# Kernel optimization log

Hardware: AMD Instinct MI355X
Metric: run time of the kernel (lower is better)

## Reference

```python
import jax, jax.numpy as jnp
import numpy as np

B, S, D = 2, 2048, 1024
H, HD = 16, 64

def setup_inputs() -> dict:
    key = jax.random.key(0)
    k1, k2, k3 = jax.random.split(key, 3)
    x = jax.random.normal(k1, (B, S, D), dtype=jnp.float32)
    w_qkv = jax.random.normal(k2, (3 * D, D), dtype=jnp.float32) * (D ** -0.5)
    w_out = jax.random.normal(k3, (D, D), dtype=jnp.float32) * (D ** -0.5)
    return {"x": x, "w_qkv": w_qkv, "w_out": w_out}

def reference(x, w_qkv, w_out):
    scale = HD ** -0.5
    # qkv projection: torch Linear applies x @ W.T
    qkv = jnp.einsum('bsd,ed->bse', x, w_qkv)            # [B,S,3D]
    qkv = qkv.reshape(B, S, 3, H, HD)
    q, k, v = qkv[:, :, 0], qkv[:, :, 1], qkv[:, :, 2]   # [B,S,H,HD]
    # scores: explicit matmul-softmax-matmul (unfused, as in source)
    scores = jnp.einsum('bqhd,bkhd->bhqk', q, k) * scale  # [B,H,S,S]
    attn = jax.nn.softmax(scores, axis=-1)
    out = jnp.einsum('bhqk,bkhd->bqhd', attn, v)          # [B,S,H,HD]
    out = out.reshape(B, S, D)
    return jnp.einsum('bsd,ed->bse', out, w_out)
```

## Files before the change

### kernel.cpp

```cpp
#include <hip/hip_runtime.h>
#include <math.h>

#define B_ 2
#define S_ 2048
#define D_ 1024
#define H_ 16
#define HD_ 64

typedef short bf16x8 __attribute__((ext_vector_type(8)));
typedef short bf16x4 __attribute__((ext_vector_type(4)));
typedef float f32x4 __attribute__((ext_vector_type(4)));

#define MFMA32(a, b, c) __builtin_amdgcn_mfma_f32_16x16x32_bf16(a, b, c, 0, 0, 0)
#define MFMA16(a, b, c) __builtin_amdgcn_mfma_f32_16x16x16bf16_1k(a, b, c, 0, 0, 0)

static __device__ __forceinline__ unsigned short f2bf(float f) {
    union { float f; unsigned u; } v = {f};
    return (unsigned short)((v.u + 0x7fffu + ((v.u >> 16) & 1u)) >> 16);
}

static __device__ __forceinline__ void gl2lds16(const void* g, void* l) {
    __builtin_amdgcn_global_load_lds((const __attribute__((address_space(1))) unsigned int*)g,
                                     (__attribute__((address_space(3))) unsigned int*)l,
                                     16, 0, 0);
}

__global__ __launch_bounds__(256) void cvt_all(const float* __restrict__ x,
                                               const float* __restrict__ wq,
                                               const float* __restrict__ wo,
                                               unsigned short* __restrict__ xb,
                                               unsigned short* __restrict__ wqb,
                                               unsigned short* __restrict__ wob) {
    const int N0 = 1048576, N1 = 786432, N2 = 262144;
    int stride = gridDim.x * blockDim.x;
    for (int i = blockIdx.x * blockDim.x + threadIdx.x; i < N0 + N1 + N2; i += stride) {
        const float4* src; ushort4* dst; int j;
        if (i < N0)            { src = (const float4*)x;  dst = (ushort4*)xb;  j = i; }
        else if (i < N0 + N1)  { src = (const float4*)wq; dst = (ushort4*)wqb; j = i - N0; }
        else                   { src = (const float4*)wo; dst = (ushort4*)wob; j = i - N0 - N1; }
        float4 v = src[j];
        ushort4 o;
        o.x = f2bf(v.x); o.y = f2bf(v.y); o.z = f2bf(v.z); o.w = f2bf(v.w);
        dst[j] = o;
    }
}

template <int BN>
__global__ __launch_bounds__(256) void gemm_nt_b(const unsigned short* __restrict__ A,
                                                 const unsigned short* __restrict__ Bm,
                                                 void* __restrict__ Cout,
                                                 int M, int N, int K, int c_bf16) {
    constexpr int BM = 128, BK = 32;
    constexpr int MI = (BN == 128) ? 4 : 2;
    constexpr int NI = 4;
    constexpr int SEGS = (BM + BN) / 16;
    __shared__ unsigned short As[BM * BK];
    __shared__ unsigned short Bs[BN * BK];

    const int tid = threadIdx.x;
    const int wave = tid >> 6, lane = tid & 63;
    const int m16 = lane & 15, quad = lane >> 4;
    const int wrow = (BN == 128) ? (wave >> 1) * 64 : wave * 32;
    const int wcol = (BN == 128) ? (wave & 1) * 64 : 0;
    const int row0 = blockIdx.y * BM, col0 = blockIdx.x * BN;

    const int lrow = lane >> 2;
    const int lk = (lane & 3) * 8;

    f32x4 acc[MI][NI] = {};

    for (int k0 = 0; k0 < K; k0 += BK) {
        __syncthreads();
        for (int s = wave; s < SEGS; s += 4) {
            if (s < BM / 16) {
                gl2lds16(&A[(size_t)(row0 + s * 16 + lrow) * K + k0 + lk],
                         &As[s * 16 * BK]);
            } else {
                int t = s - BM / 16;
                gl2lds16(&Bm[(size_t)(col0 + t * 16 + lrow) * K + k0 + lk],
                         &Bs[t * 16 * BK]);
            }
        }
        __asm__ volatile("s_waitcnt vmcnt(0)" ::: "memory");
        __syncthreads();

        bf16x8 af[MI], bfr[NI];
        #pragma unroll
        for (int mi = 0; mi < MI; ++mi)
            af[mi] = *(const bf16x8*)&As[(wrow + mi * 16 + m16) * BK + quad * 8];
        #pragma unroll
        for (int ni = 0; ni < NI; ++ni)
            bfr[ni] = *(const bf16x8*)&Bs[(wcol + ni * 16 + m16) * BK + quad * 8];
        #pragma unroll
        for (int mi = 0; mi < MI; ++mi)
            #pragma unroll
            for (int ni = 0; ni < NI; ++ni)
                acc[mi][ni] = MFMA32(af[mi], bfr[ni], acc[mi][ni]);
    }

    #pragma unroll
    for (int mi = 0; mi < MI; ++mi) {
        #pragma unroll
        for (int r = 0; r < 4; ++r) {
            size_t grow = row0 + wrow + mi * 16 + quad * 4 + r;
            #pragma unroll
            for (int ni = 0; ni < NI; ++ni) {
                size_t gcol = col0 + wcol + ni * 16 + m16;
                if (c_bf16)
                    ((unsigned short*)Cout)[grow * N + gcol] = f2bf(acc[mi][ni][r]);
                else
                    ((float*)Cout)[grow * N + gcol] = acc[mi][ni][r];
            }
        }
    }
}

__global__ __launch_bounds__(256) void attn_mfma(const unsigned short* __restrict__ qkv,
                                                 unsigned short* __restrict__ out) {
    constexpr int LDK = 72;
    __shared__ unsigned short Ks[2][64 * LDK];
    __shared__ unsigned short Vt[2][64 * LDK];

    const int id = blockIdx.x;
    const int bh = ((id >> 3) & 3) * 8 + (id & 7);
    const int b = bh >> 4, h = bh & 15;
    const int q0 = (id >> 5) * 64;

    const int tid = threadIdx.x;
    const int wave = tid >> 6, lane = tid & 63;
    const int m16 = lane & 15, quad = lane >> 4;

    const float C1 = 0.125f * 1.44269504089f;
    const float C2 = 10.0f * 1.44269504089f;

    const unsigned short* qrow =
        qkv + ((size_t)b * S_ + q0 + wave * 16 + m16) * (3 * D_) + h * HD_;
    bf16x8 qf0 = *(const bf16x8*)(qrow + quad * 8);
    bf16x8 qf1 = *(const bf16x8*)(qrow + 32 + quad * 8);

    f32x4 o[4] = {};
    f32x4 ol = {0.f, 0.f, 0.f, 0.f};
    const bf16x4 onesf = {(short)0x3F80, (short)0x3F80, (short)0x3F80, (short)0x3F80};

    const unsigned short* kbase = qkv + (size_t)b * S_ * 3 * D_ + D_ + h * HD_;
    const unsigned short* vbase = qkv + (size_t)b * S_ * 3 * D_ + 2 * D_ + h * HD_;

    const int kr = tid >> 3;
    const int kc8 = (tid & 7) * 8;
    const int vrp = (tid >> 4) * 2;
    const int vc4 = (tid & 15) * 4;
    const int vxr = 4 * ((tid & 15) & 7);

    int vaddr[4][4];
    #pragma unroll
    for (int dt = 0; dt < 4; ++dt) {
        int d = dt * 16 + m16;
        int xr = 4 * ((d >> 2) & 7);
        #pragma unroll
        for (int nt = 0; nt < 4; ++nt)
            vaddr[dt][nt] = d * LDK + ((nt * 16 + quad * 4) ^ xr);
    }

    uint4 kg[2];
    ushort4 vg[2][2];

    #pragma unroll
    for (int i = 0; i < 2; ++i) {
        kg[i] = *(const uint4*)(kbase + (size_t)(kr + i * 32) * 3 * D_ + kc8);
        vg[i][0] = *(const ushort4*)(vbase + (size_t)(vrp + i * 32) * 3 * D_ + vc4);
        vg[i][1] = *(const ushort4*)(vbase + (size_t)(vrp + i * 32 + 1) * 3 * D_ + vc4);
    }
    #pragma unroll
    for (int i = 0; i < 2; ++i) {
        *(uint4*)&Ks[0][(kr + i * 32) * LDK + kc8] = kg[i];
        int koff = (vrp + i * 32) ^ vxr;
        *(unsigned*)&Vt[0][(vc4 + 0) * LDK + koff] = (unsigned)vg[i][0].x | ((unsigned)vg[i][1].x << 16);
        *(unsigned*)&Vt[0][(vc4 + 1) * LDK + koff] = (unsigned)vg[i][0].y | ((unsigned)vg[i][1].y << 16);
        *(unsigned*)&Vt[0][(vc4 + 2) * LDK + koff] = (unsigned)vg[i][0].z | ((unsigned)vg[i][1].z << 16);
        *(unsigned*)&Vt[0][(vc4 + 3) * LDK + koff] = (unsigned)vg[i][0].w | ((unsigned)vg[i][1].w << 16);
    }
    __syncthreads();

    for (int t = 0; t < S_ / 64; ++t) {
        const int buf = t & 1;
        const bool more = (t + 1) < (S_ / 64);

        if (more) {
            const size_t kt1 = (size_t)(t + 1) * 64;
            #pragma unroll
            for (int i = 0; i < 2; ++i) {
                kg[i] = *(const uint4*)(kbase + (kt1 + kr + i * 32) * 3 * D_ + kc8);
                vg[i][0] = *(const ushort4*)(vbase + (kt1 + vrp + i * 32) * 3 * D_ + vc4);
                vg[i][1] = *(const ushort4*)(vbase + (kt1 + vrp + i * 32 + 1) * 3 * D_ + vc4);
            }
        }

        bf16x4 pf[4];
        #pragma unroll
        for (int nt = 0; nt < 4; ++nt) {
            const unsigned short* kp = &Ks[buf][(nt * 16 + m16) * LDK];
            bf16x8 kf0 = *(const bf16x8*)(kp + quad * 8);
            bf16x8 kf1 = *(const bf16x8*)(kp + 32 + quad * 8);
            f32x4 z = {0.f, 0.f, 0.f, 0.f};
            z = MFMA32(kf0, qf0, z);
            z = MFMA32(kf1, qf1, z);
            float p0 = __builtin_amdgcn_exp2f(z[0] * C1 - C2);
            float p1 = __builtin_amdgcn_exp2f(z[1] * C1 - C2);
            float p2 = __builtin_amdgcn_exp2f(z[2] * C1 - C2);
            float p3 = __builtin_amdgcn_exp2f(z[3] * C1 - C2);
            union { float f; unsigned u; } u0 = {p0}, u1 = {p1}, u2 = {p2}, u3 = {p3};
            unsigned lo = __builtin_amdgcn_perm(u1.u + 0x8000u, u0.u + 0x8000u, 0x07060302u);
            unsigned hi = __builtin_amdgcn_perm(u3.u + 0x8000u, u2.u + 0x8000u, 0x07060302u);
            union { unsigned u[2]; bf16x4 v; } pk;
            pk.u[0] = lo; pk.u[1] = hi;
            pf[nt] = pk.v;
            ol = MFMA16(pf[nt], onesf, ol);
        }

        #pragma unroll
        for (int nt = 0; nt < 4; ++nt)
            #pragma unroll
            for (int dt = 0; dt < 4; ++dt) {
                bf16x4 vf = *(const bf16x4*)&Vt[buf][vaddr[dt][nt]];
                o[dt] = MFMA16(pf[nt], vf, o[dt]);
            }

        if (more) {
            #pragma unroll
            for (int i = 0; i < 2; ++i) {
                *(uint4*)&Ks[buf ^ 1][(kr + i * 32) * LDK + kc8] = kg[i];
                int koff = (vrp + i * 32) ^ vxr;
                *(unsigned*)&Vt[buf ^ 1][(vc4 + 0) * LDK + koff] = (unsigned)vg[i][0].x | ((unsigned)vg[i][1].x << 16);
                *(unsigned*)&Vt[buf ^ 1][(vc4 + 1) * LDK + koff] = (unsigned)vg[i][0].y | ((unsigned)vg[i][1].y << 16);
                *(unsigned*)&Vt[buf ^ 1][(vc4 + 2) * LDK + koff] = (unsigned)vg[i][0].z | ((unsigned)vg[i][1].z << 16);
                *(unsigned*)&Vt[buf ^ 1][(vc4 + 3) * LDK + koff] = (unsigned)vg[i][0].w | ((unsigned)vg[i][1].w << 16);
            }
        }
        __syncthreads();
    }

    #pragma unroll
    for (int r = 0; r < 4; ++r) {
        float inv = 1.f / ol[r];
        size_t row = (size_t)b * S_ + q0 + wave * 16 + quad * 4 + r;
        unsigned short* op = out + row * D_ + h * HD_;
        #pragma unroll
        for (int dt = 0; dt < 4; ++dt)
            op[dt * 16 + m16] = f2bf(o[dt][r] * inv);
    }
}

extern "C" void kernel_launch(void* const* d_in, const int* in_sizes, int n_in,
                              void* d_out, int out_size, void* d_ws, size_t ws_size,
                              hipStream_t stream) {
    const float* x     = (const float*)d_in[0];
    const float* w_qkv = (const float*)d_in[1];
    const float* w_out = (const float*)d_in[2];
    float* out = (float*)d_out;

    const size_t n_x = (size_t)B_ * S_ * D_;
    const size_t n_wqkv = (size_t)3 * D_ * D_;
    const size_t n_wout = (size_t)D_ * D_;

    unsigned short* xb    = (unsigned short*)d_ws;
    unsigned short* wqkvb = xb + n_x;
    unsigned short* woutb = wqkvb + n_wqkv;
    unsigned short* qkvb  = woutb + n_wout;
    unsigned short* attnb = qkvb + (size_t)B_ * S_ * 3 * D_;

    dim3 blk(256);

    cvt_all<<<2048, blk, 0, stream>>>(x, w_qkv, w_out, xb, wqkvb, woutb);

    gemm_nt_b<128><<<dim3(3 * D_ / 128, B_ * S_ / 128), blk, 0, stream>>>(
        xb, wqkvb, qkvb, B_ * S_, 3 * D_, D_, 1);

    attn_mfma<<<1024, blk, 0, stream>>>(qkvb, attnb);

    gemm_nt_b<64><<<dim3(D_ / 64, B_ * S_ / 128), blk, 0, stream>>>(
        attnb, woutb, out, B_ * S_, D_, D_, 0);
}
```

Baseline: 214.9 us.

## Load K fragments directly from global memory into registers, skipping LDS staging

The attention kernel drops the shared-memory K tile and has each wave load its K MFMA fragments straight from global memory into registers at the start of every iteration. This removes the LDS writes and reads for K and shrinks shared-memory use. The cost is that all four waves in a block redundantly fetch the same K rows, and those loads are no longer prefetched a tile ahead, so their latency sits directly in front of the QK MFMAs. The P-to-bf16 packing also switches from a hand-written perm trick to the HIP __float22bfloat162_rn intrinsic.

```diff
diff --git a/kernel.cpp b/kernel.cpp
--- a/kernel.cpp
+++ b/kernel.cpp
@@ -1,4 +1,5 @@
 #include <hip/hip_runtime.h>
+#include <hip/hip_bf16.h>
 #include <math.h>
 
 #define B_ 2
@@ -17,6 +18,13 @@
 static __device__ __forceinline__ unsigned short f2bf(float f) {
     union { float f; unsigned u; } v = {f};
     return (unsigned short)((v.u + 0x7fffu + ((v.u >> 16) & 1u)) >> 16);
+}
+
+static __device__ __forceinline__ unsigned pk2bf(float a, float b) {
+    __hip_bfloat162 h = __float22bfloat162_rn(make_float2(a, b));
+    unsigned r;
+    __builtin_memcpy(&r, &h, 4);
+    return r;
 }
 
 static __device__ __forceinline__ void gl2lds16(const void* g, void* l) {
@@ -118,7 +126,6 @@
 __global__ __launch_bounds__(256) void attn_mfma(const unsigned short* __restrict__ qkv,
                                                  unsigned short* __restrict__ out) {
     constexpr int LDK = 72;
-    __shared__ unsigned short Ks[2][64 * LDK];
     __shared__ unsigned short Vt[2][64 * LDK];
 
     const int id = blockIdx.x;
@@ -145,8 +152,8 @@
     const unsigned short* kbase = qkv + (size_t)b * S_ * 3 * D_ + D_ + h * HD_;
     const unsigned short* vbase = qkv + (size_t)b * S_ * 3 * D_ + 2 * D_ + h * HD_;
 
-    const int kr = tid >> 3;
-    const int kc8 = (tid & 7) * 8;
+    const unsigned short* kfp = kbase + (size_t)m16 * (3 * D_) + quad * 8;
+
     const int vrp = (tid >> 4) * 2;
     const int vc4 = (tid & 15) * 4;
     const int vxr = 4 * ((tid & 15) & 7);
@@ -161,18 +168,15 @@
             vaddr[dt][nt] = d * LDK + ((nt * 16 + quad * 4) ^ xr);
     }
 
-    uint4 kg[2];
     ushort4 vg[2][2];
 
     #pragma unroll
     for (int i = 0; i < 2; ++i) {
-        kg[i] = *(const uint4*)(kbase + (size_t)(kr + i * 32) * 3 * D_ + kc8);
         vg[i][0] = *(const ushort4*)(vbase + (size_t)(vrp + i * 32) * 3 * D_ + vc4);
         vg[i][1] = *(const ushort4*)(vbase + (size_t)(vrp + i * 32 + 1) * 3 * D_ + vc4);
     }
     #pragma unroll
     for (int i = 0; i < 2; ++i) {
-        *(uint4*)&Ks[0][(kr + i * 32) * LDK + kc8] = kg[i];
         int koff = (vrp + i * 32) ^ vxr;
         *(unsigned*)&Vt[0][(vc4 + 0) * LDK + koff] = (unsigned)vg[i][0].x | ((unsigned)vg[i][1].x << 16);
         *(unsigned*)&Vt[0][(vc4 + 1) * LDK + koff] = (unsigned)vg[i][0].y | ((unsigned)vg[i][1].y << 16);
@@ -185,11 +189,18 @@
         const int buf = t & 1;
         const bool more = (t + 1) < (S_ / 64);
 
+        uint4 kf[8];
+        #pragma unroll
+        for (int nt = 0; nt < 4; ++nt) {
+            const unsigned short* kp = kfp + (size_t)(t * 64 + nt * 16) * (3 * D_);
+            kf[nt * 2 + 0] = *(const uint4*)kp;
+            kf[nt * 2 + 1] = *(const uint4*)(kp + 32);
+        }
+
         if (more) {
             const size_t kt1 = (size_t)(t + 1) * 64;
             #pragma unroll
             for (int i = 0; i < 2; ++i) {
-                kg[i] = *(const uint4*)(kbase + (kt1 + kr + i * 32) * 3 * D_ + kc8);
                 vg[i][0] = *(const ushort4*)(vbase + (kt1 + vrp + i * 32) * 3 * D_ + vc4);
                 vg[i][1] = *(const ushort4*)(vbase + (kt1 + vrp + i * 32 + 1) * 3 * D_ + vc4);
             }
@@ -198,9 +209,9 @@
         bf16x4 pf[4];
         #pragma unroll
         for (int nt = 0; nt < 4; ++nt) {
-            const unsigned short* kp = &Ks[buf][(nt * 16 + m16) * LDK];
-            bf16x8 kf0 = *(const bf16x8*)(kp + quad * 8);
-            bf16x8 kf1 = *(const bf16x8*)(kp + 32 + quad * 8);
+            bf16x8 kf0, kf1;
+            __builtin_memcpy(&kf0, &kf[nt * 2 + 0], 16);
+            __builtin_memcpy(&kf1, &kf[nt * 2 + 1], 16);
             f32x4 z = {0.f, 0.f, 0.f, 0.f};
             z = MFMA32(kf0, qf0, z);
             z = MFMA32(kf1, qf1, z);
@@ -208,11 +219,9 @@
             float p1 = __builtin_amdgcn_exp2f(z[1] * C1 - C2);
             float p2 = __builtin_amdgcn_exp2f(z[2] * C1 - C2);
             float p3 = __builtin_amdgcn_exp2f(z[3] * C1 - C2);
-            union { float f; unsigned u; } u0 = {p0}, u1 = {p1}, u2 = {p2}, u3 = {p3};
-            unsigned lo = __builtin_amdgcn_perm(u1.u + 0x8000u, u0.u + 0x8000u, 0x07060302u);
-            unsigned hi = __builtin_amdgcn_perm(u3.u + 0x8000u, u2.u + 0x8000u, 0x07060302u);
             union { unsigned u[2]; bf16x4 v; } pk;
-            pk.u[0] = lo; pk.u[1] = hi;
+            pk.u[0] = pk2bf(p0, p1);
+            pk.u[1] = pk2bf(p2, p3);
             pf[nt] = pk.v;
             ol = MFMA16(pf[nt], onesf, ol);
         }
@@ -228,7 +237,6 @@
         if (more) {
             #pragma unroll
             for (int i = 0; i < 2; ++i) {
-                *(uint4*)&Ks[buf ^ 1][(kr + i * 32) * LDK + kc8] = kg[i];
                 int koff = (vrp + i * 32) ^ vxr;
                 *(unsigned*)&Vt[buf ^ 1][(vc4 + 0) * LDK + koff] = (unsigned)vg[i][0].x | ((unsigned)vg[i][1].x << 16);
                 *(unsigned*)&Vt[buf ^ 1][(vc4 + 1) * LDK + koff] = (unsigned)vg[i][0].y | ((unsigned)vg[i][1].y << 16);
```

Result: slower. 285.2 us (+32.7%).
